# Kernel optimization log

Hardware: AMD Instinct MI355X
Metric: run time of the kernel (lower is better)

Reference implementation:

```python
import jax, jax.numpy as jnp
import numpy as np

B = 256        # batch size
D = 256        # feature dim
N = 100000     # memory bank size (num pseudo classes)
TEMP = 0.07    # SCT_Memory temperature


def setup_inputs() -> dict:
    key = jax.random.key(0)
    k1, k2, k3 = jax.random.split(key, 3)
    inputs = jax.random.normal(k1, (B, D), dtype=jnp.float32)
    # ReID features are L2-normalized before hitting the memory
    inputs = inputs / jnp.linalg.norm(inputs, axis=1, keepdims=True)
    indexes = jax.random.randint(k2, (B,), 0, N, dtype=jnp.int32)
    features = jax.random.normal(k3, (N, D), dtype=jnp.float32)
    features = features / jnp.linalg.norm(features, axis=1, keepdims=True)
    return {"inputs": inputs, "indexes": indexes, "features": features,
            "momentum": 0.2}


def reference(inputs, indexes, features, momentum):
    # ExemplarMemory.forward: outputs = inputs.mm(features.t())
    # SCT_Memory then scales by 1/temp to form cluster_score.
    out = jnp.matmul(inputs, features.T)  # [B, N]
    return out / TEMP
```

## Files before the change

### kernel.cpp

```cpp
#include <hip/hip_runtime.h>
#include <hip/hip_bf16.h>


typedef __attribute__((ext_vector_type(8)))  __bf16 bf16x8;
typedef __attribute__((ext_vector_type(4)))  float  floatx4;
typedef __attribute__((ext_vector_type(4)))  unsigned int uint4v;

#define NB 100000
#define KD 256
#define MB 256
#define BN 64
#define LDS_STRIDE 132

union FragCast { uint4v u; bf16x8 f; };

__device__ __forceinline__ unsigned pk(float a, float b) {
  __hip_bfloat162 h = __float22bfloat162_rn(float2{a, b});
  union { __hip_bfloat162 h2; unsigned u; } cvt;
  cvt.h2 = h;
  return cvt.u;
}

__global__ __launch_bounds__(512, 4)
void sct_memory_gemm(const float* __restrict__ inputs,
                     const float* __restrict__ features,
                     float* __restrict__ out) {
  __shared__ unsigned lds[BN * LDS_STRIDE];

  const int tid = threadIdx.x;
  const int n0 = blockIdx.x * BN;

  #pragma unroll
  for (int i = 0; i < 4; ++i) {
    const int c  = i * 512 + tid;
    const int r  = c >> 5;
    const int ck = c & 31;
    const int n  = n0 + r;
    float4 f0 = make_float4(0.f, 0.f, 0.f, 0.f), f1 = f0;
    if (n < NB) {
      const float4* p =
          reinterpret_cast<const float4*>(features + (size_t)n * KD + ck * 8);
      f0 = p[0];
      f1 = p[1];
    }
    uint4v w;
    w.x = pk(f0.x, f0.y); w.y = pk(f0.z, f0.w);
    w.z = pk(f1.x, f1.y); w.w = pk(f1.z, f1.w);
    *reinterpret_cast<uint4v*>(&lds[r * LDS_STRIDE + ck * 4]) = w;
  }

  const int wave  = tid >> 6;
  const int lane  = tid & 63;
  const int lquad = lane >> 4;
  const int l16   = lane & 15;

  bf16x8 afrag[2][8];
  #pragma unroll
  for (int s = 0; s < 2; ++s) {
    const int m = wave * 32 + s * 16 + l16;
    const float* arow = inputs + (size_t)m * KD + lquad * 8;
    #pragma unroll
    for (int t = 0; t < 8; ++t) {
      const float4* p = reinterpret_cast<const float4*>(arow + t * 32);
      const float4 a0 = p[0], a1 = p[1];
      FragCast fc;
      fc.u.x = pk(a0.x, a0.y); fc.u.y = pk(a0.z, a0.w);
      fc.u.z = pk(a1.x, a1.y); fc.u.w = pk(a1.z, a1.w);
      afrag[s][t] = fc.f;
    }
  }

  __syncthreads();

  floatx4 acc[2][4];
  #pragma unroll
  for (int s = 0; s < 2; ++s)
    #pragma unroll
    for (int nt = 0; nt < 4; ++nt)
      acc[s][nt] = floatx4{0.f, 0.f, 0.f, 0.f};

  #pragma unroll
  for (int t = 0; t < 8; ++t) {
    bf16x8 bfrag[4];
    #pragma unroll
    for (int nt = 0; nt < 4; ++nt) {
      const int row = nt * 16 + l16;
      FragCast fc;
      fc.u = *reinterpret_cast<const uint4v*>(
          &lds[row * LDS_STRIDE + t * 16 + lquad * 4]);
      bfrag[nt] = fc.f;
    }
    #pragma unroll
    for (int s = 0; s < 2; ++s)
      #pragma unroll
      for (int nt = 0; nt < 4; ++nt)
        acc[s][nt] = __builtin_amdgcn_mfma_f32_16x16x32_bf16(
            afrag[s][t], bfrag[nt], acc[s][nt], 0, 0, 0);
  }

  const float scale = 1.0f / 0.07f;
  #pragma unroll
  for (int s = 0; s < 2; ++s) {
    const int mbase = wave * 32 + s * 16 + lquad * 4;
    #pragma unroll
    for (int nt = 0; nt < 4; ++nt) {
      const int n = n0 + nt * 16 + l16;
      if (n < NB) {
        #pragma unroll
        for (int r = 0; r < 4; ++r) {
          out[(size_t)(mbase + r) * NB + n] = acc[s][nt][r] * scale;
        }
      }
    }
  }
}

extern "C" void kernel_launch(void* const* d_in, const int* in_sizes, int n_in,
                              void* d_out, int out_size, void* d_ws, size_t ws_size,
                              hipStream_t stream) {
  const float* inputs   = (const float*)d_in[0];
  const float* features = (const float*)d_in[2];
  float* out = (float*)d_out;

  const int grid = (NB + BN - 1) / BN;
  sct_memory_gemm<<<grid, 512, 0, stream>>>(inputs, features, out);
}
```

Measured before the change: 236.3 us.

## Use persistent 1024-thread blocks with register prefetch of next feature tile

Replaces the one-block-per-64-row-tile launch with a persistent grid of 256 blocks of 1024 threads that loop over N tiles. Each block converts the A fragments once, prefetches the next tile's features into registers while computing the current one, and folds the 1/temperature scale into the bf16 A operand. It also switches the output index math to 32-bit. The aim is to cut per-block setup and A reloads and to overlap global loads with MFMA work. The costs are extra barriers per tile, fewer resident waves, and a small rounding change from scaling before the bf16 conversion.

Result: faster. 200.2 us (-15.3%).

```diff
diff --git a/kernel.cpp b/kernel.cpp
--- a/kernel.cpp
+++ b/kernel.cpp
@@ -2,114 +2,126 @@
 #include <hip/hip_bf16.h>
 
 
-typedef __attribute__((ext_vector_type(8)))  __bf16 bf16x8;
-typedef __attribute__((ext_vector_type(4)))  float  floatx4;
-typedef __attribute__((ext_vector_type(4)))  unsigned int uint4v;
+typedef __attribute__((ext_vector_type(8))) __bf16 bf16x8;
+typedef __attribute__((ext_vector_type(4))) float  floatx4;
+typedef __attribute__((ext_vector_type(4))) unsigned int uint4v;
 
 #define NB 100000
 #define KD 256
-#define MB 256
 #define BN 64
+#define NTILES 1563
+#define GRID 256
 #define LDS_STRIDE 132
 
 union FragCast { uint4v u; bf16x8 f; };
 
 __device__ __forceinline__ unsigned pk(float a, float b) {
   __hip_bfloat162 h = __float22bfloat162_rn(float2{a, b});
-  union { __hip_bfloat162 h2; unsigned u; } cvt;
-  cvt.h2 = h;
-  return cvt.u;
+  union { __hip_bfloat162 h2; unsigned u; } c; c.h2 = h; return c.u;
 }
 
-__global__ __launch_bounds__(512, 4)
-void sct_memory_gemm(const float* __restrict__ inputs,
-                     const float* __restrict__ features,
-                     float* __restrict__ out) {
+__global__ __launch_bounds__(1024, 4)
+void sct_gemm(const float* __restrict__ inputs,
+              const float* __restrict__ features,
+              float* __restrict__ out) {
   __shared__ unsigned lds[BN * LDS_STRIDE];
 
-  const int tid = threadIdx.x;
-  const int n0 = blockIdx.x * BN;
+  const int tid  = threadIdx.x;
+  const int ws   = tid >> 6;
+  const int lane = tid & 63;
+  const int quad = lane >> 4;
+  const int l16  = lane & 15;
 
-  #pragma unroll
-  for (int i = 0; i < 4; ++i) {
-    const int c  = i * 512 + tid;
-    const int r  = c >> 5;
-    const int ck = c & 31;
-    const int n  = n0 + r;
-    float4 f0 = make_float4(0.f, 0.f, 0.f, 0.f), f1 = f0;
-    if (n < NB) {
-      const float4* p =
-          reinterpret_cast<const float4*>(features + (size_t)n * KD + ck * 8);
-      f0 = p[0];
-      f1 = p[1];
+  const int b = blockIdx.x;
+  const int ntiles = (NTILES - b + GRID - 1) / GRID;
+
+  const int srow0 = tid >> 5,            sck0 = tid & 31;
+  const int srow1 = (1024 + tid) >> 5,   sck1 = tid & 31;
+
+  float4 pf0a, pf0b, pf1a, pf1b;
+  {
+    const int n0 = b * BN;
+    pf0a = pf0b = pf1a = pf1b = make_float4(0.f, 0.f, 0.f, 0.f);
+    if (n0 + srow0 < NB) {
+      const float4* p = (const float4*)(features + (size_t)(n0 + srow0) * KD + sck0 * 8);
+      pf0a = p[0]; pf0b = p[1];
     }
-    uint4v w;
-    w.x = pk(f0.x, f0.y); w.y = pk(f0.z, f0.w);
-    w.z = pk(f1.x, f1.y); w.w = pk(f1.z, f1.w);
-    *reinterpret_cast<uint4v*>(&lds[r * LDS_STRIDE + ck * 4]) = w;
-  }
-
-  const int wave  = tid >> 6;
-  const int lane  = tid & 63;
-  const int lquad = lane >> 4;
-  const int l16   = lane & 15;
-
-  bf16x8 afrag[2][8];
-  #pragma unroll
-  for (int s = 0; s < 2; ++s) {
-    const int m = wave * 32 + s * 16 + l16;
-    const float* arow = inputs + (size_t)m * KD + lquad * 8;
-    #pragma unroll
-    for (int t = 0; t < 8; ++t) {
-      const float4* p = reinterpret_cast<const float4*>(arow + t * 32);
-      const float4 a0 = p[0], a1 = p[1];
-      FragCast fc;
-      fc.u.x = pk(a0.x, a0.y); fc.u.y = pk(a0.z, a0.w);
-      fc.u.z = pk(a1.x, a1.y); fc.u.w = pk(a1.z, a1.w);
-      afrag[s][t] = fc.f;
+    if (n0 + srow1 < NB) {
+      const float4* p = (const float4*)(features + (size_t)(n0 + srow1) * KD + sck1 * 8);
+      pf1a = p[0]; pf1b = p[1];
     }
   }
 
-  __syncthreads();
-
-  floatx4 acc[2][4];
-  #pragma unroll
-  for (int s = 0; s < 2; ++s)
+  const float scale = 1.0f / 0.07f;
+  bf16x8 afrag[8];
+  {
+    const float* arow = inputs + (ws * 16 + l16) * KD + quad * 8;
     #pragma unroll
-    for (int nt = 0; nt < 4; ++nt)
-      acc[s][nt] = floatx4{0.f, 0.f, 0.f, 0.f};
-
-  #pragma unroll
-  for (int t = 0; t < 8; ++t) {
-    bf16x8 bfrag[4];
-    #pragma unroll
-    for (int nt = 0; nt < 4; ++nt) {
-      const int row = nt * 16 + l16;
+    for (int t = 0; t < 8; ++t) {
+      const float4* p = (const float4*)(arow + t * 32);
+      const float4 a0 = p[0], a1 = p[1];
       FragCast fc;
-      fc.u = *reinterpret_cast<const uint4v*>(
-          &lds[row * LDS_STRIDE + t * 16 + lquad * 4]);
-      bfrag[nt] = fc.f;
+      fc.u.x = pk(a0.x * scale, a0.y * scale);
+      fc.u.y = pk(a0.z * scale, a0.w * scale);
+      fc.u.z = pk(a1.x * scale, a1.y * scale);
+      fc.u.w = pk(a1.z * scale, a1.w * scale);
+      afrag[t] = fc.f;
     }
-    #pragma unroll
-    for (int s = 0; s < 2; ++s)
-      #pragma unroll
-      for (int nt = 0; nt < 4; ++nt)
-        acc[s][nt] = __builtin_amdgcn_mfma_f32_16x16x32_bf16(
-            afrag[s][t], bfrag[nt], acc[s][nt], 0, 0, 0);
   }
 
-  const float scale = 1.0f / 0.07f;
-  #pragma unroll
-  for (int s = 0; s < 2; ++s) {
-    const int mbase = wave * 32 + s * 16 + lquad * 4;
+  const unsigned obase = (unsigned)((ws * 16 + quad * 4) * NB + l16);
+
+  for (int it = 0; it < ntiles; ++it) {
+    const int n0 = (b + it * GRID) * BN;
+
+    __syncthreads();
+
+    {
+      uint4v w;
+      w.x = pk(pf0a.x, pf0a.y); w.y = pk(pf0a.z, pf0a.w);
+      w.z = pk(pf0b.x, pf0b.y); w.w = pk(pf0b.z, pf0b.w);
+      *(uint4v*)&lds[srow0 * LDS_STRIDE + sck0 * 4] = w;
+      w.x = pk(pf1a.x, pf1a.y); w.y = pk(pf1a.z, pf1a.w);
+      w.z = pk(pf1b.x, pf1b.y); w.w = pk(pf1b.z, pf1b.w);
+      *(uint4v*)&lds[srow1 * LDS_STRIDE + sck1 * 4] = w;
+    }
+    __syncthreads();
+
+    if (it + 1 < ntiles) {
+      const int nn0 = (b + (it + 1) * GRID) * BN;
+      pf0a = pf0b = pf1a = pf1b = make_float4(0.f, 0.f, 0.f, 0.f);
+      if (nn0 + srow0 < NB) {
+        const float4* p = (const float4*)(features + (size_t)(nn0 + srow0) * KD + sck0 * 8);
+        pf0a = p[0]; pf0b = p[1];
+      }
+      if (nn0 + srow1 < NB) {
+        const float4* p = (const float4*)(features + (size_t)(nn0 + srow1) * KD + sck1 * 8);
+        pf1a = p[0]; pf1b = p[1];
+      }
+    }
+
+    floatx4 acc[4];
+    #pragma unroll
+    for (int nt = 0; nt < 4; ++nt) acc[nt] = floatx4{0.f, 0.f, 0.f, 0.f};
+
+    #pragma unroll
+    for (int t = 0; t < 8; ++t) {
+      #pragma unroll
+      for (int nt = 0; nt < 4; ++nt) {
+        FragCast fc;
+        fc.u = *(const uint4v*)&lds[(nt * 16 + l16) * LDS_STRIDE + t * 16 + quad * 4];
+        acc[nt] = __builtin_amdgcn_mfma_f32_16x16x32_bf16(afrag[t], fc.f, acc[nt], 0, 0, 0);
+      }
+    }
+
     #pragma unroll
     for (int nt = 0; nt < 4; ++nt) {
       const int n = n0 + nt * 16 + l16;
       if (n < NB) {
+        const unsigned col = obase + (unsigned)(n0 + nt * 16);
         #pragma unroll
-        for (int r = 0; r < 4; ++r) {
-          out[(size_t)(mbase + r) * NB + n] = acc[s][nt][r] * scale;
-        }
+        for (int r = 0; r < 4; ++r)
+          out[col + (unsigned)(r * NB)] = acc[nt][r];
       }
     }
   }
@@ -122,6 +134,5 @@
   const float* features = (const float*)d_in[2];
   float* out = (float*)d_out;
 
-  const int grid = (NB + BN - 1) / BN;
-  sct_memory_gemm<<<grid, 512, 0, stream>>>(inputs, features, out);
+  sct_gemm<<<GRID, 1024, 0, stream>>>(inputs, features, out);
 }
```
